# Performance work log

Measured on AMD Instinct MI355X. Metric: run time of the kernel, lower is better.

## Reference

```python
import jax, jax.numpy as jnp
import numpy as np
import math

B, L, E, H = 512, 200, 64, 4
D = E // H
NEG = jnp.float32(-(2.0 ** 32) + 1.0)


def setup_inputs() -> dict:
    key = jax.random.key(0)
    ks = jax.random.split(key, 12)
    inp = jax.random.normal(ks[0], (B, L, E), dtype=jnp.float32)
    # realistic variable-length histories: mask[b, t] = t < len_b, len_b in [1, L]
    lens = jax.random.randint(ks[1], (B, 1), 1, L + 1)
    mask = jnp.arange(L)[None, :] < lens  # [B, L] bool
    s = 1.0 / math.sqrt(E)
    pos_enc = jax.random.normal(ks[2], (1, L, E), dtype=jnp.float32)
    Wk = jax.random.uniform(ks[3], (E, E), jnp.float32, -s, s)
    bk = jnp.zeros((E,), jnp.float32)
    Wv = jax.random.uniform(ks[4], (E, E), jnp.float32, -s, s)
    bv = jnp.zeros((E,), jnp.float32)
    Wq = jax.random.uniform(ks[5], (E, E), jnp.float32, -s, s)
    bq = jnp.zeros((E,), jnp.float32)
    Wf = jax.random.uniform(ks[6], (E, E), jnp.float32, -s, s)
    bf = jnp.zeros((E,), jnp.float32)
    return {"input": inp, "mask": mask, "pos_enc": pos_enc,
            "Wk": Wk, "bk": bk, "Wv": Wv, "bv": bv,
            "Wq": Wq, "bq": bq, "Wf": Wf, "bf": bf}


def reference(input, mask, pos_enc, Wk, bk, Wv, bv, Wq, bq, Wf, bf):
    x = input + pos_enc  # [B, L, E]
    # project and split heads: [B, H, L, D]
    def split(t):
        return t.reshape(B, L, H, D).transpose(0, 2, 1, 3)
    k = split(x @ Wk.T + bk)
    v = split(x @ Wv.T + bv)
    q = split(x @ Wq.T + bq) / math.sqrt(D)
    scores = jnp.einsum('bhqd,bhkd->bhqk', q, k)  # [B, H, L, L]
    # key_mask in torch code broadcasts over dim 3 (mask on the QUERY axis),
    # query_mask is its transpose (mask on the KEY axis). Combined: both must be valid.
    both = mask[:, None, :, None] & mask[:, None, None, :]  # [B, 1, L, L]
    scores = jnp.where(both, scores, NEG)
    attn = jax.nn.softmax(scores, axis=-1)
    # dropout is identity at inference; omitted deterministically
    out = jnp.einsum('bhqk,bhkd->bhqd', attn, v)
    out = out.transpose(0, 2, 1, 3).reshape(B, L, E)
    out = out @ Wf.T + bf
    fm = mask.astype(jnp.float32)[:, :, None]  # [B, L, 1]
    lens = jnp.sum(fm, axis=1)  # [B, 1]
    pooled = jnp.sum(out * fm, axis=1) / (lens + 1e-8)  # [B, E]
    return pooled
```

## Files before the change

### kernel.cpp

```cpp
#include <hip/hip_runtime.h>
#include <hip/hip_fp16.h>
#include <math.h>

#define Bn 512
#define Ln 200
#define En 64
#define Hn 4
#define Dn 16
#define KS3 18
#define VS3 200
#define QSC 0.36067376022224085f

typedef _Float16 __f16;
typedef __f16 f16x4 __attribute__((ext_vector_type(4)));
typedef __f16 f16x8 __attribute__((ext_vector_type(8)));
typedef float f32x4 __attribute__((ext_vector_type(4)));

#if __has_builtin(__builtin_amdgcn_exp2f)
__device__ __forceinline__ float fexp2(float x) { return __builtin_amdgcn_exp2f(x); }
#else
__device__ __forceinline__ float fexp2(float x) { return exp2f(x); }
#endif

__device__ __forceinline__ f16x8 pack8s(float4 a, float4 b, float4 pa, float4 pb) {
    f16x8 r;
    r[0] = (__f16)(a.x + pa.x); r[1] = (__f16)(a.y + pa.y);
    r[2] = (__f16)(a.z + pa.z); r[3] = (__f16)(a.w + pa.w);
    r[4] = (__f16)(b.x + pb.x); r[5] = (__f16)(b.y + pb.y);
    r[6] = (__f16)(b.z + pb.z); r[7] = (__f16)(b.w + pb.w);
    return r;
}
__device__ __forceinline__ f16x8 pack8(float4 a, float4 b) {
    f16x8 r;
    r[0] = (__f16)a.x; r[1] = (__f16)a.y; r[2] = (__f16)a.z; r[3] = (__f16)a.w;
    r[4] = (__f16)b.x; r[5] = (__f16)b.y; r[6] = (__f16)b.z; r[7] = (__f16)b.w;
    return r;
}

__global__ __launch_bounds__(256, 6) void fused_kernel(
    const float* __restrict__ input, const int* __restrict__ mask,
    const float* __restrict__ pos_enc,
    const float* __restrict__ Wk, const float* __restrict__ bk,
    const float* __restrict__ Wv, const float* __restrict__ bv,
    const float* __restrict__ Wq, const float* __restrict__ bq,
    const float* __restrict__ Wf, const float* __restrict__ bf_,
    float* __restrict__ out)
{
    __shared__ __align__(16) __f16 Kh[Ln * KS3];
    __shared__ __align__(16) __f16 Qh[Ln * KS3];
    __shared__ __align__(16) __f16 Vt[16 * VS3];
    __shared__ float lred[4][4][16];
    __shared__ float red[4][16];
    __shared__ float ph[16];
    __shared__ int cnt_red[4];

    const int tid  = threadIdx.x;
    const int b    = blockIdx.x >> 2, h = blockIdx.x & 3;
    const int wave = tid >> 6, lane = tid & 63;
    const int quad = lane >> 4, ln16 = lane & 15;

    const int mv = (tid < Ln) ? mask[b * Ln + tid] : 0;

    f16x8 bfr[3][2];
    #pragma unroll
    for (int m = 0; m < 3; ++m) {
        const float* W = (m == 0) ? Wk : (m == 1) ? Wv : Wq;
        #pragma unroll
        for (int ks = 0; ks < 2; ++ks) {
            const float4* wp = (const float4*)(W + (size_t)(h * 16 + ln16) * 64) + (ks * 8 + quad * 2);
            bfr[m][ks] = pack8(wp[0], wp[1]);
        }
    }
    const int cg = h * 16 + ln16;
    const float bkv = bk[cg], bvv = bv[cg], bqv = bq[cg];

    int c = (mv != 0) ? 1 : 0;
    #pragma unroll
    for (int off = 32; off; off >>= 1) c += __shfl_down(c, off, 64);
    if (lane == 0) cnt_red[wave] = c;
    __syncthreads();
    const int len = cnt_red[0] + cnt_red[1] + cnt_red[2] + cnt_red[3];
    const int nt = (len + 15) >> 4;

    const float4* in4 = (const float4*)(input + (size_t)b * Ln * En);
    const float4* pe4 = (const float4*)pos_enc;

    for (int rt = wave; rt < nt; rt += 4) {
        const int R = rt * 16 + ln16;
        const bool rok = (R < Ln);
        f16x8 af[2];
        #pragma unroll
        for (int ks = 0; ks < 2; ++ks) {
            float4 xa = {0,0,0,0}, xb = {0,0,0,0}, pa = {0,0,0,0}, pb = {0,0,0,0};
            if (rok) {
                const int o4 = R * 16 + ks * 8 + quad * 2;
                xa = in4[o4]; xb = in4[o4 + 1];
                pa = pe4[o4]; pb = pe4[o4 + 1];
            }
            af[ks] = pack8s(xa, xb, pa, pb);
        }
        f32x4 acc[3];
        #pragma unroll
        for (int m = 0; m < 3; ++m) acc[m] = (f32x4){0,0,0,0};
        #pragma unroll
        for (int ks = 0; ks < 2; ++ks)
            #pragma unroll
            for (int m = 0; m < 3; ++m)
                acc[m] = __builtin_amdgcn_mfma_f32_16x16x32_f16(af[ks], bfr[m][ks], acc[m], 0, 0, 0);

        #pragma unroll
        for (int j = 0; j < 4; ++j) {
            const int t = rt * 16 + quad * 4 + j;
            if (t < Ln) {
                Kh[t * KS3 + ln16] = (__f16)(acc[0][j] + bkv);
                Qh[t * KS3 + ln16] = (__f16)((acc[2][j] + bqv) * QSC);
            }
        }
        const int vc0 = rt * 16 + quad * 4;
        if (vc0 < Ln) {
            f16x4 vp;
            #pragma unroll
            for (int j = 0; j < 4; ++j) vp[j] = (__f16)(acc[1][j] + bvv);
            *(f16x4*)(Vt + ln16 * VS3 + vc0) = vp;
        }
    }
    __syncthreads();

    const int nquad = (nt + 3) >> 2;
    int g, kh, nkh;
    if (nquad >= 3)      { g = wave;     kh = 0;         nkh = 1; }
    else if (nquad == 2) { g = wave & 1; kh = wave >> 1; nkh = 2; }
    else                 { g = 0;        kh = wave;      nkh = 4; }
    const bool active = (g < nquad);
    const int nktp = (nt + nkh - 1) / nkh;
    const int klo = kh * nktp;
    const int khi = min(klo + nktp, nt);
    const int qt0 = 4 * g;

    f32x4 o2[4];
    float l[4] = {0.f, 0.f, 0.f, 0.f};
    #pragma unroll
    for (int i = 0; i < 4; ++i) o2[i] = (f32x4){0,0,0,0};

    if (active && klo < khi) {
        f16x4 qf[4];
        #pragma unroll
        for (int i = 0; i < 4; ++i) {
            int qr = min((qt0 + i) * 16 + ln16, Ln - 1);
            qf[i] = *(const f16x4*)(Qh + qr * KS3 + quad * 4);
        }
        f16x4 kf = *(const f16x4*)(Kh + min(klo * 16 + ln16, Ln - 1) * KS3 + quad * 4);
        f16x4 vf = *(const f16x4*)(Vt + ln16 * VS3 + min(klo * 16 + quad * 4, Ln - 4));

        for (int kt = klo; kt < khi; ++kt) {
            const int krn = min((kt + 1) * 16 + ln16, Ln - 1);
            const int vcn = min((kt + 1) * 16 + quad * 4, Ln - 4);
            const f16x4 kfn = *(const f16x4*)(Kh + krn * KS3 + quad * 4);
            const f16x4 vfn = *(const f16x4*)(Vt + ln16 * VS3 + vcn);
            const int kbase = kt * 16 + quad * 4;
            f32x4 s[4];
            #pragma unroll
            for (int i = 0; i < 4; ++i)
                s[i] = __builtin_amdgcn_mfma_f32_16x16x16f16(kf, qf[i], (f32x4){0,0,0,0}, 0, 0, 0);
            f16x4 pf[4];
            #pragma unroll
            for (int i = 0; i < 4; ++i) {
                #pragma unroll
                for (int j = 0; j < 4; ++j) {
                    const bool kok = (kbase + j) < len;
                    float p = kok ? fexp2(fminf(s[i][j], 14.5f)) : 0.f;
                    l[i] += p;
                    pf[i][j] = (__f16)p;
                }
            }
            #pragma unroll
            for (int i = 0; i < 4; ++i)
                o2[i] = __builtin_amdgcn_mfma_f32_16x16x16f16(vf, pf[i], o2[i], 0, 0, 0);
            kf = kfn; vf = vfn;
        }
        #pragma unroll
        for (int i = 0; i < 4; ++i) {
            l[i] += __shfl_xor(l[i], 16, 64);
            l[i] += __shfl_xor(l[i], 32, 64);
        }
    }

    if (lane < 16) {
        #pragma unroll
        for (int i = 0; i < 4; ++i) lred[wave][i][lane] = l[i];
    }
    __syncthreads();

    f32x4 pool = {0.f, 0.f, 0.f, 0.f};
    if (active) {
        #pragma unroll
        for (int i = 0; i < 4; ++i) {
            float lt;
            if (nkh == 1)      lt = lred[wave][i][ln16];
            else if (nkh == 2) lt = lred[g][i][ln16] + lred[g + 2][i][ln16];
            else               lt = lred[0][i][ln16] + lred[1][i][ln16]
                                  + lred[2][i][ln16] + lred[3][i][ln16];
            const float rs = ((qt0 + i) * 16 + ln16 < len) ? 1.f / lt : 0.f;
            #pragma unroll
            for (int j = 0; j < 4; ++j) pool[j] = fmaf(o2[i][j], rs, pool[j]);
        }
    }

    #pragma unroll
    for (int j = 0; j < 4; ++j) {
        #pragma unroll
        for (int off = 1; off < 16; off <<= 1) pool[j] += __shfl_xor(pool[j], off, 64);
    }
    if (ln16 == 0) {
        #pragma unroll
        for (int j = 0; j < 4; ++j) red[wave][quad * 4 + j] = pool[j];
    }
    __syncthreads();
    if (tid < 16)
        ph[tid] = (red[0][tid] + red[1][tid] + red[2][tid] + red[3][tid]) / ((float)len + 1e-8f);
    __syncthreads();

    if (tid < 64) {
        const int e = tid;
        const float* wr = Wf + (size_t)e * 64 + h * 16;
        float a = (h == 0) ? bf_[e] : 0.f;
        #pragma unroll
        for (int i = 0; i < 16; ++i) a = fmaf(wr[i], ph[i], a);
        atomicAdd(out + b * En + e, a);
    }
}

extern "C" void kernel_launch(void* const* d_in, const int* in_sizes, int n_in,
                              void* d_out, int out_size, void* d_ws, size_t ws_size,
                              hipStream_t stream) {
    const float* input   = (const float*)d_in[0];
    const int*   mask    = (const int*)  d_in[1];
    const float* pos_enc = (const float*)d_in[2];
    const float* Wk      = (const float*)d_in[3];
    const float* bk      = (const float*)d_in[4];
    const float* Wv      = (const float*)d_in[5];
    const float* bv      = (const float*)d_in[6];
    const float* Wq      = (const float*)d_in[7];
    const float* bq      = (const float*)d_in[8];
    const float* Wf      = (const float*)d_in[9];
    const float* bf      = (const float*)d_in[10];

    float* out = (float*)d_out;
    hipMemsetAsync(out, 0, (size_t)Bn * En * sizeof(float), stream);

    fused_kernel<<<Bn * Hn, 256, 0, stream>>>(input, mask, pos_enc,
                                              Wk, bk, Wv, bv, Wq, bq, Wf, bf, out);
}
```

Before: 123.7 us.

## Compute softmax row sums with MFMA against ones and peel masked last tile

Row-sum accumulation of exponentiated scores moves from scalar adds plus cross-lane shuffles to an extra MFMA that multiplies the probabilities by a ones vector. The last key tile is peeled, so key masking runs only where keys can exceed the length and the main loop skips per-element compares. The shared-memory reduction and its barrier are now skipped when a single wave owns a query group. Launch bounds drop from 6 to 4 waves per SIMD to allow more registers, which may lower occupancy.

```diff
diff --git a/kernel.cpp b/kernel.cpp
--- a/kernel.cpp
+++ b/kernel.cpp
@@ -37,7 +37,7 @@
     return r;
 }
 
-__global__ __launch_bounds__(256, 6) void fused_kernel(
+__global__ __launch_bounds__(256, 4) void fused_kernel(
     const float* __restrict__ input, const int* __restrict__ mask,
     const float* __restrict__ pos_enc,
     const float* __restrict__ Wk, const float* __restrict__ bk,
@@ -137,10 +137,10 @@
     const int khi = min(klo + nktp, nt);
     const int qt0 = 4 * g;
 
-    f32x4 o2[4];
-    float l[4] = {0.f, 0.f, 0.f, 0.f};
-    #pragma unroll
-    for (int i = 0; i < 4; ++i) o2[i] = (f32x4){0,0,0,0};
+    const f16x4 ones = {(__f16)1.f, (__f16)1.f, (__f16)1.f, (__f16)1.f};
+    f32x4 o2[4], lacc[4];
+    #pragma unroll
+    for (int i = 0; i < 4; ++i) { o2[i] = (f32x4){0,0,0,0}; lacc[i] = (f32x4){0,0,0,0}; }
 
     if (active && klo < khi) {
         f16x4 qf[4];
@@ -149,15 +149,17 @@
             int qr = min((qt0 + i) * 16 + ln16, Ln - 1);
             qf[i] = *(const f16x4*)(Qh + qr * KS3 + quad * 4);
         }
+        const bool needmask = (khi == nt);
+        const int kfull = khi - (needmask ? 1 : 0);
+
         f16x4 kf = *(const f16x4*)(Kh + min(klo * 16 + ln16, Ln - 1) * KS3 + quad * 4);
         f16x4 vf = *(const f16x4*)(Vt + ln16 * VS3 + min(klo * 16 + quad * 4, Ln - 4));
 
-        for (int kt = klo; kt < khi; ++kt) {
+        for (int kt = klo; kt < kfull; ++kt) {
             const int krn = min((kt + 1) * 16 + ln16, Ln - 1);
             const int vcn = min((kt + 1) * 16 + quad * 4, Ln - 4);
             const f16x4 kfn = *(const f16x4*)(Kh + krn * KS3 + quad * 4);
             const f16x4 vfn = *(const f16x4*)(Vt + ln16 * VS3 + vcn);
-            const int kbase = kt * 16 + quad * 4;
             f32x4 s[4];
             #pragma unroll
             for (int i = 0; i < 4; ++i)
@@ -166,41 +168,62 @@
             #pragma unroll
             for (int i = 0; i < 4; ++i) {
                 #pragma unroll
+                for (int j = 0; j < 4; ++j)
+                    pf[i][j] = (__f16)fexp2(fminf(s[i][j], 14.5f));
+            }
+            #pragma unroll
+            for (int i = 0; i < 4; ++i) {
+                o2[i]   = __builtin_amdgcn_mfma_f32_16x16x16f16(vf,   pf[i], o2[i],   0, 0, 0);
+                lacc[i] = __builtin_amdgcn_mfma_f32_16x16x16f16(ones, pf[i], lacc[i], 0, 0, 0);
+            }
+            kf = kfn; vf = vfn;
+        }
+        if (needmask) {
+            const int kbase = (nt - 1) * 16 + quad * 4;
+            f32x4 s[4];
+            #pragma unroll
+            for (int i = 0; i < 4; ++i)
+                s[i] = __builtin_amdgcn_mfma_f32_16x16x16f16(kf, qf[i], (f32x4){0,0,0,0}, 0, 0, 0);
+            f16x4 pf[4];
+            #pragma unroll
+            for (int i = 0; i < 4; ++i) {
+                #pragma unroll
                 for (int j = 0; j < 4; ++j) {
                     const bool kok = (kbase + j) < len;
-                    float p = kok ? fexp2(fminf(s[i][j], 14.5f)) : 0.f;
-                    l[i] += p;
-                    pf[i][j] = (__f16)p;
+                    pf[i][j] = kok ? (__f16)fexp2(fminf(s[i][j], 14.5f)) : (__f16)0.f;
                 }
             }
             #pragma unroll
-            for (int i = 0; i < 4; ++i)
-                o2[i] = __builtin_amdgcn_mfma_f32_16x16x16f16(vf, pf[i], o2[i], 0, 0, 0);
-            kf = kfn; vf = vfn;
-        }
+            for (int i = 0; i < 4; ++i) {
+                o2[i]   = __builtin_amdgcn_mfma_f32_16x16x16f16(vf,   pf[i], o2[i],   0, 0, 0);
+                lacc[i] = __builtin_amdgcn_mfma_f32_16x16x16f16(ones, pf[i], lacc[i], 0, 0, 0);
+            }
+        }
+    }
+
+    float l[4];
+    #pragma unroll
+    for (int i = 0; i < 4; ++i) l[i] = lacc[i][0];
+
+    if (nkh > 1) {
+        if (lane < 16) {
+            #pragma unroll
+            for (int i = 0; i < 4; ++i) lred[wave][i][lane] = l[i];
+        }
+        __syncthreads();
         #pragma unroll
         for (int i = 0; i < 4; ++i) {
-            l[i] += __shfl_xor(l[i], 16, 64);
-            l[i] += __shfl_xor(l[i], 32, 64);
-        }
-    }
-
-    if (lane < 16) {
-        #pragma unroll
-        for (int i = 0; i < 4; ++i) lred[wave][i][lane] = l[i];
-    }
-    __syncthreads();
+            if (nkh == 2) l[i] = lred[g][i][ln16] + lred[g + 2][i][ln16];
+            else          l[i] = lred[0][i][ln16] + lred[1][i][ln16]
+                               + lred[2][i][ln16] + lred[3][i][ln16];
+        }
+    }
 
     f32x4 pool = {0.f, 0.f, 0.f, 0.f};
     if (active) {
         #pragma unroll
         for (int i = 0; i < 4; ++i) {
-            float lt;
-            if (nkh == 1)      lt = lred[wave][i][ln16];
-            else if (nkh == 2) lt = lred[g][i][ln16] + lred[g + 2][i][ln16];
-            else               lt = lred[0][i][ln16] + lred[1][i][ln16]
-                                  + lred[2][i][ln16] + lred[3][i][ln16];
-            const float rs = ((qt0 + i) * 16 + ln16 < len) ? 1.f / lt : 0.f;
+            const float rs = ((qt0 + i) * 16 + ln16 < len) ? 1.f / l[i] : 0.f;
             #pragma unroll
             for (int j = 0; j < 4; ++j) pool[j] = fmaf(o2[i][j], rs, pool[j]);
         }
```

After: 122.3 us. No clear change (-1.1%).
